# Optimization experiments

Measured on AMD Instinct MI355X. Metric: run time of the kernel, lower is better.

The kernel has to match this reference:

```python
import jax, jax.numpy as jnp
import numpy as np

NODELEN = 394
N_NODES = 50000
N_EDGES = 200000
IN_DIM = 2 * NODELEN  # 788
H2 = 192
EMB = 128


def setup_inputs() -> dict:
    key = jax.random.key(0)
    ks = jax.random.split(key, 12)
    inp = {
        'features': jax.random.normal(ks[0], (N_NODES, NODELEN), dtype=jnp.float32),
        'src': jax.random.randint(ks[1], (N_EDGES,), 0, N_NODES),
        'dst': jax.random.randint(ks[2], (N_EDGES,), 0, N_NODES),
        # AutoEncoder params (Linear weights stored as [in, out])
        'W_enc1': jax.random.normal(ks[3], (IN_DIM, H2), dtype=jnp.float32) / np.sqrt(IN_DIM),
        'b_enc1': jnp.zeros((H2,), dtype=jnp.float32),
        'W_enc3': jax.random.normal(ks[4], (H2, EMB), dtype=jnp.float32) / np.sqrt(H2),
        'b_enc3': jnp.zeros((EMB,), dtype=jnp.float32),
        'W_dec1': jax.random.normal(ks[5], (EMB, H2), dtype=jnp.float32) / np.sqrt(EMB),
        'b_dec1': jnp.zeros((H2,), dtype=jnp.float32),
        'W_dec3': jax.random.normal(ks[6], (H2, IN_DIM), dtype=jnp.float32) / np.sqrt(H2),
        'b_dec3': jnp.zeros((IN_DIM,), dtype=jnp.float32),
    }
    return inp


def _segment_mean(msgs, dst, inv_deg, n):
    # msgs: [E, F] gathered neighbor features; mean over incoming edges per node
    return jax.ops.segment_sum(msgs, dst, num_segments=n) * inv_deg


def reference(features, src, dst, W_enc1, b_enc1, W_enc3, b_enc3,
              W_dec1, b_dec1, W_dec3, b_dec3):
    n = features.shape[0]
    ones = jnp.ones(src.shape[0], dtype=features.dtype)
    deg = jax.ops.segment_sum(ones, dst, num_segments=n)
    # nodes with no neighbors fall back to the zero dummy vector (as in source)
    inv_deg = (1.0 / jnp.maximum(deg, 1.0))[:, None]

    # depth-1 aggregation: mean of raw neighbor features, then feat[0] := 0
    h1 = _segment_mean(features[src], dst, inv_deg, n)
    h1 = h1.at[:, 0].set(0.0)
    # depth-2 aggregation: mean of depth-1 aggregates of neighbors, feat[0] := 0
    h2 = _segment_mean(h1[src], dst, inv_deg, n)
    h2 = h2.at[:, 0].set(0.0)

    # concatenated embedding with positions 0 and NODELEN zeroed
    emb = jnp.concatenate([features, h2], axis=1)  # [N, 788]
    emb = emb.at[:, 0].set(0.0).at[:, NODELEN].set(0.0)

    # AutoEncoder forward (dropout is identity at inference)
    x = jax.nn.relu(emb @ W_enc1 + b_enc1)
    encoded = x @ W_enc3 + b_enc3
    y = jax.nn.relu(encoded @ W_dec1 + b_dec1)
    decoded = y @ W_dec3 + b_dec3
    return encoded, decoded, emb
```

## Files before the change

kernel.cpp:

```cpp
#include <hip/hip_runtime.h>
#include <hip/hip_bf16.h>

#define NODELEN 394
#define IN_DIM 788
#define H2DIM 192
#define EMBDIM 128
#define NCHUNK 197

typedef __attribute__((ext_vector_type(4))) float f32x4;
typedef __attribute__((ext_vector_type(8))) short bfrag;

static __device__ __forceinline__ unsigned short f2bf(float f) {
    union { float f; unsigned u; } v; v.f = f;
    unsigned r = v.u + 0x7FFFu + ((v.u >> 16) & 1u);
    return (unsigned short)(r >> 16);
}
static __device__ __forceinline__ float bf2f(unsigned short h) {
    union { unsigned u; float f; } v; v.u = ((unsigned)h) << 16;
    return v.f;
}


__global__ void count_deg(const int* __restrict__ dst, int* __restrict__ deg, int e) {
    int i = blockIdx.x * blockDim.x + threadIdx.x;
    if (i < e) atomicAdd(&deg[dst[i]], 1);
}

__global__ void block_sum(const int* __restrict__ deg, int* __restrict__ bsum, int n) {
    __shared__ int s[256];
    int t = threadIdx.x;
    int i = blockIdx.x * 256 + t;
    s[t] = (i < n) ? deg[i] : 0;
    __syncthreads();
    for (int d = 128; d > 0; d >>= 1) {
        if (t < d) s[t] += s[t + d];
        __syncthreads();
    }
    if (t == 0) bsum[blockIdx.x] = s[0];
}

__global__ void scan_bsums(int* bsum, int nb) {
    __shared__ int s[256];
    int t = threadIdx.x;
    int x0 = (t < nb) ? bsum[t] : 0;
    s[t] = x0;
    __syncthreads();
    for (int d = 1; d < 256; d <<= 1) {
        int u = (t >= d) ? s[t - d] : 0;
        __syncthreads();
        s[t] += u;
        __syncthreads();
    }
    if (t < nb) bsum[t] = s[t] - x0;
}

__global__ void block_scan(const int* __restrict__ deg, const int* __restrict__ boff,
                           int* __restrict__ rowstart, int* __restrict__ cursor,
                           float* __restrict__ inv, int n) {
    __shared__ int s[256];
    int t = threadIdx.x;
    int i = blockIdx.x * 256 + t;
    int x0 = (i < n) ? deg[i] : 0;
    s[t] = x0;
    __syncthreads();
    for (int d = 1; d < 256; d <<= 1) {
        int u = (t >= d) ? s[t - d] : 0;
        __syncthreads();
        s[t] += u;
        __syncthreads();
    }
    if (i < n) {
        int r = boff[blockIdx.x] + s[t] - x0;
        rowstart[i] = r;
        cursor[i] = r;
        inv[i] = 1.0f / fmaxf((float)x0, 1.0f);
    }
}

__global__ void fill_edges(const int* __restrict__ src, const int* __restrict__ dst,
                           int* __restrict__ cursor, int* __restrict__ elist, int e) {
    int i = blockIdx.x * blockDim.x + threadIdx.x;
    if (i < e) {
        int p = atomicAdd(&cursor[dst[i]], 1);
        elist[p] = src[i];
    }
}


__global__ __launch_bounds__(256) void gather1(
        const float* __restrict__ feat, const int* __restrict__ rowstart,
        const int* __restrict__ deg, const float* __restrict__ inv,
        const int* __restrict__ elist, unsigned short* __restrict__ h1) {
    const int node = blockIdx.x;
    const int c = threadIdx.x;
    if (c >= NCHUNK) return;
    const int beg = rowstart[node];
    const int dc = deg[node];
    const float s = inv[node];
    const size_t off = (size_t)c * 2;

    float ax = 0.f, ay = 0.f, bx = 0.f, by = 0.f;
    float cx = 0.f, cy = 0.f, dx = 0.f, dy = 0.f;
    int j = 0;
    for (; j + 3 < dc; j += 4) {
        int n0 = elist[beg + j], n1 = elist[beg + j + 1];
        int n2 = elist[beg + j + 2], n3 = elist[beg + j + 3];
        float2 v0 = *(const float2*)(feat + (size_t)n0 * NODELEN + off);
        float2 v1 = *(const float2*)(feat + (size_t)n1 * NODELEN + off);
        float2 v2 = *(const float2*)(feat + (size_t)n2 * NODELEN + off);
        float2 v3 = *(const float2*)(feat + (size_t)n3 * NODELEN + off);
        ax += v0.x; ay += v0.y; bx += v1.x; by += v1.y;
        cx += v2.x; cy += v2.y; dx += v3.x; dy += v3.y;
    }
    for (; j < dc; ++j) {
        int n0 = elist[beg + j];
        float2 v0 = *(const float2*)(feat + (size_t)n0 * NODELEN + off);
        ax += v0.x; ay += v0.y;
    }
    float fx = (ax + bx + cx + dx) * s;
    float fy = (ay + by + cy + dy) * s;
    if (c == 0) fx = 0.f;
    unsigned out = ((unsigned)f2bf(fy) << 16) | (unsigned)f2bf(fx);
    *(unsigned*)(h1 + (size_t)node * NODELEN + off) = out;
}

__global__ __launch_bounds__(256) void gather2_emb(
        const float* __restrict__ feat, const unsigned* __restrict__ h1,
        const int* __restrict__ rowstart, const int* __restrict__ deg,
        const float* __restrict__ inv, const int* __restrict__ elist,
        float* __restrict__ emb) {
    const int node = blockIdx.x;
    const int c = threadIdx.x;
    if (c >= NCHUNK) return;
    const int beg = rowstart[node];
    const int dc = deg[node];
    const float s = inv[node];

    float ax = 0.f, ay = 0.f, bx = 0.f, by = 0.f;
    float cx = 0.f, cy = 0.f, dx = 0.f, dy = 0.f;
    int j = 0;
    for (; j + 3 < dc; j += 4) {
        int n0 = elist[beg + j], n1 = elist[beg + j + 1];
        int n2 = elist[beg + j + 2], n3 = elist[beg + j + 3];
        unsigned u0 = h1[(size_t)n0 * NCHUNK + c];
        unsigned u1 = h1[(size_t)n1 * NCHUNK + c];
        unsigned u2 = h1[(size_t)n2 * NCHUNK + c];
        unsigned u3 = h1[(size_t)n3 * NCHUNK + c];
        ax += bf2f((unsigned short)u0); ay += bf2f((unsigned short)(u0 >> 16));
        bx += bf2f((unsigned short)u1); by += bf2f((unsigned short)(u1 >> 16));
        cx += bf2f((unsigned short)u2); cy += bf2f((unsigned short)(u2 >> 16));
        dx += bf2f((unsigned short)u3); dy += bf2f((unsigned short)(u3 >> 16));
    }
    for (; j < dc; ++j) {
        int n0 = elist[beg + j];
        unsigned u0 = h1[(size_t)n0 * NCHUNK + c];
        ax += bf2f((unsigned short)u0); ay += bf2f((unsigned short)(u0 >> 16));
    }
    float hx = (ax + bx + cx + dx) * s;
    float hy = (ay + by + cy + dy) * s;

    const float* fr = feat + (size_t)node * NODELEN;
    float* er = emb + (size_t)node * IN_DIM;
    float2 fv = *(const float2*)(fr + c * 2);
    if (c == 0) { fv.x = 0.f; hx = 0.f; }
    *(float2*)(er + c * 2) = fv;
    float2 hv; hv.x = hx; hv.y = hy;
    *(float2*)(er + NODELEN + c * 2) = hv;
}

__device__ __forceinline__ void tr_one(const float* W, unsigned short* Wt,
                                       int K, int N, int Kp, int idx) {
    int nrow = idx / Kp, k = idx - nrow * Kp;
    Wt[idx] = (k < K) ? f2bf(W[(size_t)k * N + nrow]) : (unsigned short)0;
}

#define T1E (192 * 800)
#define T2E (128 * 192)
#define T3E (192 * 128)
#define T4E (788 * 192)

__global__ void transpose_all(const float* __restrict__ W1, unsigned short* __restrict__ Wt1,
                              const float* __restrict__ W2, unsigned short* __restrict__ Wt2,
                              const float* __restrict__ W3, unsigned short* __restrict__ Wt3,
                              const float* __restrict__ W4, unsigned short* __restrict__ Wt4) {
    int idx = blockIdx.x * 256 + threadIdx.x;
    if (idx < T1E) { tr_one(W1, Wt1, IN_DIM, H2DIM, 800, idx); return; }
    idx -= T1E;
    if (idx < T2E) { tr_one(W2, Wt2, H2DIM, EMBDIM, 192, idx); return; }
    idx -= T2E;
    if (idx < T3E) { tr_one(W3, Wt3, EMBDIM, H2DIM, 128, idx); return; }
    idx -= T3E;
    if (idx < T4E) { tr_one(W4, Wt4, H2DIM, IN_DIM, 192, idx); return; }
}

static __device__ __forceinline__ int xy_base(int r, int s) {
    int ph = (s & 24) | ((s ^ r) & 7);
    return r * 192 + (ph << 3);
}
static __device__ __forceinline__ int xy_addr_s(int r, int col) { return xy_base(r, col >> 3) + (col & 7); }
static __device__ __forceinline__ int en_base(int r, int s) {
    int ph = (s & 8) | ((s ^ r) & 7);
    return r * 128 + (ph << 3);
}
static __device__ __forceinline__ int en_addr_s(int r, int col) { return en_base(r, col >> 3) + (col & 7); }

static __device__ __forceinline__ unsigned short f2bf_fast(float f) {
    __hip_bfloat16 h = __float2bfloat16(f);
    union { __hip_bfloat16 h; unsigned short u; } c; c.h = h; return c.u;
}

struct A8 { float4 a, b; };

static __device__ __forceinline__ void load_a(A8 out[2], const float* __restrict__ emb,
                                              int m0, int wm, int lr, int lk, int M, int kt) {
    int c = kt * 32 + lk * 8;
    #pragma unroll
    for (int i = 0; i < 2; ++i) {
        int gm = m0 + wm * 32 + i * 16 + lr;
        const float* rp = emb + (size_t)gm * IN_DIM;
        bool v = gm < M;
        if (v && c + 8 <= IN_DIM) {
            out[i].a = *(const float4*)(rp + c);
            out[i].b = *(const float4*)(rp + c + 4);
        } else {
            float t[8];
            #pragma unroll
            for (int q = 0; q < 8; ++q) t[q] = (v && c + q < IN_DIM) ? rp[c + q] : 0.f;
            out[i].a = make_float4(t[0], t[1], t[2], t[3]);
            out[i].b = make_float4(t[4], t[5], t[6], t[7]);
        }
    }
}

static __device__ __forceinline__ bfrag cvt_a(const A8& x) {
    union { unsigned short u[8]; bfrag v; } pk;
    pk.u[0] = f2bf_fast(x.a.x); pk.u[1] = f2bf_fast(x.a.y);
    pk.u[2] = f2bf_fast(x.a.z); pk.u[3] = f2bf_fast(x.a.w);
    pk.u[4] = f2bf_fast(x.b.x); pk.u[5] = f2bf_fast(x.b.y);
    pk.u[6] = f2bf_fast(x.b.z); pk.u[7] = f2bf_fast(x.b.w);
    return pk.v;
}

__global__ __launch_bounds__(256, 3) void mlp_fused(
    const float* __restrict__ emb,
    const unsigned short* __restrict__ Wt1,
    const unsigned short* __restrict__ Wt2,
    const unsigned short* __restrict__ Wt3,
    const unsigned short* __restrict__ Wt4,
    const float* __restrict__ b1, const float* __restrict__ b2,
    const float* __restrict__ b3, const float* __restrict__ b4,
    float* __restrict__ encoded, float* __restrict__ decoded, int M)
{
    __shared__ unsigned short XY[64 * 192];
    __shared__ unsigned short EN[64 * 128];

    const int tid = threadIdx.x;
    const int wid = tid >> 6, l = tid & 63;
    const int wm = wid >> 1, wn = wid & 1;
    const int lr = l & 15, lk = l >> 4;
    const int m0 = blockIdx.x * 64;
    const bfrag zf = {0, 0, 0, 0, 0, 0, 0, 0};

    {
        f32x4 acc[2][6];
        #pragma unroll
        for (int i = 0; i < 2; ++i)
            #pragma unroll
            for (int j = 0; j < 6; ++j) acc[i][j] = (f32x4){0.f, 0.f, 0.f, 0.f};

        const unsigned short* wp[6];
        #pragma unroll
        for (int j = 0; j < 6; ++j)
            wp[j] = Wt1 + (size_t)(wn * 96 + j * 16 + lr) * 800 + lk * 8;

        #pragma unroll 5
        for (int kt = 0; kt < 25; ++kt) {
            A8 a[2];
            load_a(a, emb, m0, wm, lr, lk, M, kt);
            bfrag bf[6];
            #pragma unroll
            for (int j = 0; j < 6; ++j) bf[j] = *(const bfrag*)(wp[j] + kt * 32);
            bfrag af0 = cvt_a(a[0]), af1 = cvt_a(a[1]);
            #pragma unroll
            for (int j = 0; j < 6; ++j) {
                acc[0][j] = __builtin_amdgcn_mfma_f32_16x16x32_bf16(af0, bf[j], acc[0][j], 0, 0, 0);
                acc[1][j] = __builtin_amdgcn_mfma_f32_16x16x32_bf16(af1, bf[j], acc[1][j], 0, 0, 0);
            }
        }
        float bv[6];
        #pragma unroll
        for (int j = 0; j < 6; ++j) bv[j] = b1[wn * 96 + j * 16 + lr];
        #pragma unroll
        for (int i = 0; i < 2; ++i)
            #pragma unroll
            for (int j = 0; j < 6; ++j)
                #pragma unroll
                for (int r = 0; r < 4; ++r) {
                    int m = wm * 32 + i * 16 + lk * 4 + r;
                    int n1 = wn * 96 + j * 16 + lr;
                    XY[xy_addr_s(m, n1)] = f2bf_fast(fmaxf(acc[i][j][r] + bv[j], 0.f));
                }
    }
    __syncthreads();

    {
        bfrag af2[6][2];
        #pragma unroll
        for (int q = 0; q < 6; ++q)
            #pragma unroll
            for (int i = 0; i < 2; ++i)
                af2[q][i] = *(const bfrag*)&XY[xy_base(wm * 32 + i * 16 + lr, q * 4 + lk)];

        f32x4 acc[2][4];
        #pragma unroll
        for (int i = 0; i < 2; ++i)
            #pragma unroll
            for (int j = 0; j < 4; ++j) acc[i][j] = (f32x4){0.f, 0.f, 0.f, 0.f};

        const unsigned short* wp[4];
        #pragma unroll
        for (int j = 0; j < 4; ++j)
            wp[j] = Wt2 + (size_t)(wn * 64 + j * 16 + lr) * 192 + lk * 8;

        #pragma unroll
        for (int kt = 0; kt < 6; ++kt) {
            bfrag bf[4];
            #pragma unroll
            for (int j = 0; j < 4; ++j) bf[j] = *(const bfrag*)(wp[j] + kt * 32);
            #pragma unroll
            for (int i = 0; i < 2; ++i)
                #pragma unroll
                for (int j = 0; j < 4; ++j)
                    acc[i][j] = __builtin_amdgcn_mfma_f32_16x16x32_bf16(af2[kt][i], bf[j], acc[i][j], 0, 0, 0);
        }
        float bv[4];
        #pragma unroll
        for (int j = 0; j < 4; ++j) bv[j] = b2[wn * 64 + j * 16 + lr];
        #pragma unroll
        for (int i = 0; i < 2; ++i)
            #pragma unroll
            for (int j = 0; j < 4; ++j)
                #pragma unroll
                for (int r = 0; r < 4; ++r) {
                    int m = wm * 32 + i * 16 + lk * 4 + r;
                    int nn = wn * 64 + j * 16 + lr;
                    float v = acc[i][j][r] + bv[j];
                    int gm = m0 + m;
                    if (gm < M) encoded[(size_t)gm * EMBDIM + nn] = v;
                    EN[en_addr_s(m, nn)] = f2bf_fast(v);
                }
    }
    __syncthreads();

    {
        bfrag af3[4][2];
        #pragma unroll
        for (int q = 0; q < 4; ++q)
            #pragma unroll
            for (int i = 0; i < 2; ++i)
                af3[q][i] = *(const bfrag*)&EN[en_base(wm * 32 + i * 16 + lr, q * 4 + lk)];

        f32x4 acc[2][6];
        #pragma unroll
        for (int i = 0; i < 2; ++i)
            #pragma unroll
            for (int j = 0; j < 6; ++j) acc[i][j] = (f32x4){0.f, 0.f, 0.f, 0.f};

        const unsigned short* wp[6];
        #pragma unroll
        for (int j = 0; j < 6; ++j)
            wp[j] = Wt3 + (size_t)(wn * 96 + j * 16 + lr) * 128 + lk * 8;

        #pragma unroll
        for (int kt = 0; kt < 4; ++kt) {
            bfrag bf[6];
            #pragma unroll
            for (int j = 0; j < 6; ++j) bf[j] = *(const bfrag*)(wp[j] + kt * 32);
            #pragma unroll
            for (int i = 0; i < 2; ++i)
                #pragma unroll
                for (int j = 0; j < 6; ++j)
                    acc[i][j] = __builtin_amdgcn_mfma_f32_16x16x32_bf16(af3[kt][i], bf[j], acc[i][j], 0, 0, 0);
        }
        float bv[6];
        #pragma unroll
        for (int j = 0; j < 6; ++j) bv[j] = b3[wn * 96 + j * 16 + lr];
        #pragma unroll
        for (int i = 0; i < 2; ++i)
            #pragma unroll
            for (int j = 0; j < 6; ++j)
                #pragma unroll
                for (int r = 0; r < 4; ++r) {
                    int m = wm * 32 + i * 16 + lk * 4 + r;
                    int nc = wn * 96 + j * 16 + lr;
                    XY[xy_addr_s(m, nc)] = f2bf_fast(fmaxf(acc[i][j][r] + bv[j], 0.f));
                }
    }
    __syncthreads();

    {
        bfrag af4[6][2];
        #pragma unroll
        for (int q = 0; q < 6; ++q)
            #pragma unroll
            for (int i = 0; i < 2; ++i)
                af4[q][i] = *(const bfrag*)&XY[xy_base(wm * 32 + i * 16 + lr, q * 4 + lk)];

        for (int nc = 0; nc < 7; ++nc) {
            f32x4 acc[2][4];
            #pragma unroll
            for (int i = 0; i < 2; ++i)
                #pragma unroll
                for (int j = 0; j < 4; ++j) acc[i][j] = (f32x4){0.f, 0.f, 0.f, 0.f};

            const int colb = nc * 128 + wn * 64 + lr;
            #pragma unroll
            for (int kt = 0; kt < 6; ++kt) {
                bfrag bf[4];
                #pragma unroll
                for (int j = 0; j < 4; ++j) {
                    int row = colb + j * 16;
                    bf[j] = (row < IN_DIM)
                        ? *(const bfrag*)(Wt4 + (size_t)row * 192 + kt * 32 + lk * 8) : zf;
                }
                #pragma unroll
                for (int i = 0; i < 2; ++i)
                    #pragma unroll
                    for (int j = 0; j < 4; ++j)
                        acc[i][j] = __builtin_amdgcn_mfma_f32_16x16x32_bf16(af4[kt][i], bf[j], acc[i][j], 0, 0, 0);
            }

            float bv[4];
            #pragma unroll
            for (int j = 0; j < 4; ++j) {
                int nn = colb + j * 16;
                bv[j] = (nn < IN_DIM) ? b4[nn] : 0.f;
            }
            #pragma unroll
            for (int i = 0; i < 2; ++i)
                #pragma unroll
                for (int j = 0; j < 4; ++j)
                    #pragma unroll
                    for (int r = 0; r < 4; ++r) {
                        int gm = m0 + wm * 32 + i * 16 + lk * 4 + r;
                        int nn = colb + j * 16;
                        if (gm < M && nn < IN_DIM)
                            decoded[(size_t)gm * IN_DIM + nn] = acc[i][j][r] + bv[j];
                    }
        }
    }
}


extern "C" void kernel_launch(void* const* d_in, const int* in_sizes, int n_in,
                              void* d_out, int out_size, void* d_ws, size_t ws_size,
                              hipStream_t stream) {
    const float* features = (const float*)d_in[0];
    const int*   src      = (const int*)d_in[1];
    const int*   dst      = (const int*)d_in[2];
    const float* W_enc1   = (const float*)d_in[3];
    const float* b_enc1   = (const float*)d_in[4];
    const float* W_enc3   = (const float*)d_in[5];
    const float* b_enc3   = (const float*)d_in[6];
    const float* W_dec1   = (const float*)d_in[7];
    const float* b_dec1   = (const float*)d_in[8];
    const float* W_dec3   = (const float*)d_in[9];
    const float* b_dec3   = (const float*)d_in[10];

    const int n = in_sizes[0] / NODELEN;
    const int e = in_sizes[1];

    float* encoded = (float*)d_out;
    float* decoded = encoded + (size_t)n * EMBDIM;
    float* emb     = decoded + (size_t)n * IN_DIM;

    char* ws = (char*)d_ws;
    unsigned short* h1  = (unsigned short*)(ws + 0);
    unsigned short* Wt1 = (unsigned short*)(ws + 40000000);
    unsigned short* Wt2 = (unsigned short*)(ws + 40400000);
    unsigned short* Wt3 = (unsigned short*)(ws + 40500000);
    unsigned short* Wt4 = (unsigned short*)(ws + 40600000);
    float* inv          = (float*)(ws + 41000000);
    int*   deg          = (int*)  (ws + 41200000);
    int*   rowstart     = (int*)  (ws + 41400000);
    int*   cursor       = (int*)  (ws + 41600000);
    int*   elist        = (int*)  (ws + 41800000);
    int*   bsum         = (int*)  (ws + 42600000);

    const int nb = (n + 255) / 256;
    const int eb = (e + 255) / 256;

    transpose_all<<<(T1E + T2E + T3E + T4E + 255) / 256, 256, 0, stream>>>(
        W_enc1, Wt1, W_enc3, Wt2, W_dec1, Wt3, W_dec3, Wt4);

    hipMemsetAsync(deg, 0, (size_t)n * sizeof(int), stream);
    count_deg<<<eb, 256, 0, stream>>>(dst, deg, e);
    block_sum<<<nb, 256, 0, stream>>>(deg, bsum, n);
    scan_bsums<<<1, 256, 0, stream>>>(bsum, nb);
    block_scan<<<nb, 256, 0, stream>>>(deg, bsum, rowstart, cursor, inv, n);
    fill_edges<<<eb, 256, 0, stream>>>(src, dst, cursor, elist, e);

    gather1<<<n, 256, 0, stream>>>(features, rowstart, deg, inv, elist, h1);
    gather2_emb<<<n, 256, 0, stream>>>(features, (const unsigned*)h1, rowstart, deg,
                                       inv, elist, emb);

    const int MB = (n + 63) / 64;
    mlp_fused<<<MB, 256, 0, stream>>>(emb, Wt1, Wt2, Wt3, Wt4,
                                      b_enc1, b_enc3, b_dec1, b_dec3,
                                      encoded, decoded, n);
}
```

Measured before the change: 415.3 us.

## Split fused MLP into two kernels and stage weights through double-buffered LDS

```diff
diff --git a/kernel.cpp b/kernel.cpp
--- a/kernel.cpp
+++ b/kernel.cpp
@@ -193,16 +193,14 @@
     if (idx < T4E) { tr_one(W4, Wt4, H2DIM, IN_DIM, 192, idx); return; }
 }
 
+static __device__ __forceinline__ int bs_addr(int r, int s) {
+    return r * 32 + ((s ^ ((r >> 1) & 3)) << 3);
+}
 static __device__ __forceinline__ int xy_base(int r, int s) {
     int ph = (s & 24) | ((s ^ r) & 7);
     return r * 192 + (ph << 3);
 }
 static __device__ __forceinline__ int xy_addr_s(int r, int col) { return xy_base(r, col >> 3) + (col & 7); }
-static __device__ __forceinline__ int en_base(int r, int s) {
-    int ph = (s & 8) | ((s ^ r) & 7);
-    return r * 128 + (ph << 3);
-}
-static __device__ __forceinline__ int en_addr_s(int r, int col) { return en_base(r, col >> 3) + (col & 7); }
 
 static __device__ __forceinline__ unsigned short f2bf_fast(float f) {
     __hip_bfloat16 h = __float2bfloat16(f);
@@ -241,18 +239,162 @@
     return pk.v;
 }
 
-__global__ __launch_bounds__(256, 3) void mlp_fused(
+__global__ __launch_bounds__(256, 3) void mlp12(
     const float* __restrict__ emb,
     const unsigned short* __restrict__ Wt1,
     const unsigned short* __restrict__ Wt2,
+    const float* __restrict__ b1, const float* __restrict__ b2,
+    float* __restrict__ encoded, unsigned short* __restrict__ enc16, int M)
+{
+    __shared__ unsigned short XY[64 * 192];
+    __shared__ unsigned short Bs[2][192 * 32];
+
+    const int tid = threadIdx.x;
+    const int wid = tid >> 6, l = tid & 63;
+    const int wm = wid >> 1, wn = wid & 1;
+    const int lr = l & 15, lk = l >> 4;
+    const int m0 = blockIdx.x * 64;
+
+    const int r0 = tid >> 2, s0 = tid & 3;
+    const int r1 = (tid + 256) >> 2;
+    const int r2 = (tid + 512) >> 2;
+    const int bw0 = bs_addr(r0, s0);
+    const int bw1 = bs_addr(r1, s0);
+    const int bw2 = bs_addr(r2, s0);
+    int brd6[6], brd4[4];
+    #pragma unroll
+    for (int j = 0; j < 6; ++j) brd6[j] = bs_addr(wn * 96 + j * 16 + lr, lk);
+    #pragma unroll
+    for (int j = 0; j < 4; ++j) brd4[j] = bs_addr(wn * 64 + j * 16 + lr, lk);
+
+    {
+        f32x4 acc[2][6];
+        #pragma unroll
+        for (int i = 0; i < 2; ++i)
+            #pragma unroll
+            for (int j = 0; j < 6; ++j) acc[i][j] = (f32x4){0.f, 0.f, 0.f, 0.f};
+
+        A8 aC[2], aN[2];
+        bfrag bC[3], bN[3];
+        load_a(aC, emb, m0, wm, lr, lk, M, 0);
+        bC[0] = *(const bfrag*)(Wt1 + (size_t)r0 * 800 + s0 * 8);
+        bC[1] = *(const bfrag*)(Wt1 + (size_t)r1 * 800 + s0 * 8);
+        bC[2] = *(const bfrag*)(Wt1 + (size_t)r2 * 800 + s0 * 8);
+
+        #pragma unroll 5
+        for (int kt = 0; kt < 25; ++kt) {
+            unsigned short* B = Bs[kt & 1];
+            *(bfrag*)&B[bw0] = bC[0];
+            *(bfrag*)&B[bw1] = bC[1];
+            *(bfrag*)&B[bw2] = bC[2];
+            if (kt < 24) {
+                int k0 = (kt + 1) * 32;
+                load_a(aN, emb, m0, wm, lr, lk, M, kt + 1);
+                bN[0] = *(const bfrag*)(Wt1 + (size_t)r0 * 800 + k0 + s0 * 8);
+                bN[1] = *(const bfrag*)(Wt1 + (size_t)r1 * 800 + k0 + s0 * 8);
+                bN[2] = *(const bfrag*)(Wt1 + (size_t)r2 * 800 + k0 + s0 * 8);
+            }
+            __syncthreads();
+            bfrag af0 = cvt_a(aC[0]), af1 = cvt_a(aC[1]);
+            bfrag bf[6];
+            #pragma unroll
+            for (int j = 0; j < 6; ++j) bf[j] = *(const bfrag*)&B[brd6[j]];
+            #pragma unroll
+            for (int j = 0; j < 6; ++j) {
+                acc[0][j] = __builtin_amdgcn_mfma_f32_16x16x32_bf16(af0, bf[j], acc[0][j], 0, 0, 0);
+                acc[1][j] = __builtin_amdgcn_mfma_f32_16x16x32_bf16(af1, bf[j], acc[1][j], 0, 0, 0);
+            }
+            if (kt < 24) {
+                aC[0] = aN[0]; aC[1] = aN[1];
+                bC[0] = bN[0]; bC[1] = bN[1]; bC[2] = bN[2];
+            }
+        }
+        float bv[6];
+        #pragma unroll
+        for (int j = 0; j < 6; ++j) bv[j] = b1[wn * 96 + j * 16 + lr];
+        #pragma unroll
+        for (int i = 0; i < 2; ++i)
+            #pragma unroll
+            for (int j = 0; j < 6; ++j)
+                #pragma unroll
+                for (int r = 0; r < 4; ++r) {
+                    int m = wm * 32 + i * 16 + lk * 4 + r;
+                    int n1 = wn * 96 + j * 16 + lr;
+                    XY[xy_addr_s(m, n1)] = f2bf_fast(fmaxf(acc[i][j][r] + bv[j], 0.f));
+                }
+    }
+    __syncthreads();
+
+    {
+        bfrag af2[6][2];
+        #pragma unroll
+        for (int q = 0; q < 6; ++q)
+            #pragma unroll
+            for (int i = 0; i < 2; ++i)
+                af2[q][i] = *(const bfrag*)&XY[xy_base(wm * 32 + i * 16 + lr, q * 4 + lk)];
+
+        f32x4 acc[2][4];
+        #pragma unroll
+        for (int i = 0; i < 2; ++i)
+            #pragma unroll
+            for (int j = 0; j < 4; ++j) acc[i][j] = (f32x4){0.f, 0.f, 0.f, 0.f};
+
+        bfrag bC[2], bN[2];
+        bC[0] = *(const bfrag*)(Wt2 + (size_t)r0 * 192 + s0 * 8);
+        bC[1] = *(const bfrag*)(Wt2 + (size_t)r1 * 192 + s0 * 8);
+
+        #pragma unroll
+        for (int kt = 0; kt < 6; ++kt) {
+            unsigned short* B = Bs[kt & 1];
+            *(bfrag*)&B[bw0] = bC[0];
+            *(bfrag*)&B[bw1] = bC[1];
+            if (kt < 5) {
+                int k0 = (kt + 1) * 32;
+                bN[0] = *(const bfrag*)(Wt2 + (size_t)r0 * 192 + k0 + s0 * 8);
+                bN[1] = *(const bfrag*)(Wt2 + (size_t)r1 * 192 + k0 + s0 * 8);
+            }
+            __syncthreads();
+            bfrag bf[4];
+            #pragma unroll
+            for (int j = 0; j < 4; ++j) bf[j] = *(const bfrag*)&B[brd4[j]];
+            #pragma unroll
+            for (int i = 0; i < 2; ++i)
+                #pragma unroll
+                for (int j = 0; j < 4; ++j)
+                    acc[i][j] = __builtin_amdgcn_mfma_f32_16x16x32_bf16(af2[kt][i], bf[j], acc[i][j], 0, 0, 0);
+            if (kt < 5) { bC[0] = bN[0]; bC[1] = bN[1]; }
+        }
+
+        float bv[4];
+        #pragma unroll
+        for (int j = 0; j < 4; ++j) bv[j] = b2[wn * 64 + j * 16 + lr];
+        #pragma unroll
+        for (int i = 0; i < 2; ++i)
+            #pragma unroll
+            for (int j = 0; j < 4; ++j)
+                #pragma unroll
+                for (int r = 0; r < 4; ++r) {
+                    int m = wm * 32 + i * 16 + lk * 4 + r;
+                    int nn = wn * 64 + j * 16 + lr;
+                    float v = acc[i][j][r] + bv[j];
+                    int gm = m0 + m;
+                    if (gm < M) {
+                        encoded[(size_t)gm * EMBDIM + nn] = v;
+                        enc16[(size_t)gm * EMBDIM + nn] = f2bf_fast(v);
+                    }
+                }
+    }
+}
+
+__global__ __launch_bounds__(256, 3) void mlp34(
+    const unsigned short* __restrict__ enc16,
     const unsigned short* __restrict__ Wt3,
     const unsigned short* __restrict__ Wt4,
-    const float* __restrict__ b1, const float* __restrict__ b2,
     const float* __restrict__ b3, const float* __restrict__ b4,
-    float* __restrict__ encoded, float* __restrict__ decoded, int M)
+    float* __restrict__ decoded, int M)
 {
     __shared__ unsigned short XY[64 * 192];
-    __shared__ unsigned short EN[64 * 128];
+    __shared__ unsigned short Bs[2][192 * 32];
 
     const int tid = threadIdx.x;
     const int wid = tid >> 6, l = tid & 63;
@@ -261,104 +403,26 @@
     const int m0 = blockIdx.x * 64;
     const bfrag zf = {0, 0, 0, 0, 0, 0, 0, 0};
 
-    {
-        f32x4 acc[2][6];
-        #pragma unroll
-        for (int i = 0; i < 2; ++i)
-            #pragma unroll
-            for (int j = 0; j < 6; ++j) acc[i][j] = (f32x4){0.f, 0.f, 0.f, 0.f};
-
-        const unsigned short* wp[6];
-        #pragma unroll
-        for (int j = 0; j < 6; ++j)
-            wp[j] = Wt1 + (size_t)(wn * 96 + j * 16 + lr) * 800 + lk * 8;
-
-        #pragma unroll 5
-        for (int kt = 0; kt < 25; ++kt) {
-            A8 a[2];
-            load_a(a, emb, m0, wm, lr, lk, M, kt);
-            bfrag bf[6];
-            #pragma unroll
-            for (int j = 0; j < 6; ++j) bf[j] = *(const bfrag*)(wp[j] + kt * 32);
-            bfrag af0 = cvt_a(a[0]), af1 = cvt_a(a[1]);
-            #pragma unroll
-            for (int j = 0; j < 6; ++j) {
-                acc[0][j] = __builtin_amdgcn_mfma_f32_16x16x32_bf16(af0, bf[j], acc[0][j], 0, 0, 0);
-                acc[1][j] = __builtin_amdgcn_mfma_f32_16x16x32_bf16(af1, bf[j], acc[1][j], 0, 0, 0);
-            }
-        }
-        float bv[6];
-        #pragma unroll
-        for (int j = 0; j < 6; ++j) bv[j] = b1[wn * 96 + j * 16 + lr];
-        #pragma unroll
-        for (int i = 0; i < 2; ++i)
-            #pragma unroll
-            for (int j = 0; j < 6; ++j)
-                #pragma unroll
-                for (int r = 0; r < 4; ++r) {
-                    int m = wm * 32 + i * 16 + lk * 4 + r;
-                    int n1 = wn * 96 + j * 16 + lr;
-                    XY[xy_addr_s(m, n1)] = f2bf_fast(fmaxf(acc[i][j][r] + bv[j], 0.f));
-                }
-    }
-    __syncthreads();
-
-    {
-        bfrag af2[6][2];
-        #pragma unroll
-        for (int q = 0; q < 6; ++q)
-            #pragma unroll
-            for (int i = 0; i < 2; ++i)
-                af2[q][i] = *(const bfrag*)&XY[xy_base(wm * 32 + i * 16 + lr, q * 4 + lk)];
-
-        f32x4 acc[2][4];
-        #pragma unroll
-        for (int i = 0; i < 2; ++i)
-            #pragma unroll
-            for (int j = 0; j < 4; ++j) acc[i][j] = (f32x4){0.f, 0.f, 0.f, 0.f};
-
-        const unsigned short* wp[4];
-        #pragma unroll
-        for (int j = 0; j < 4; ++j)
-            wp[j] = Wt2 + (size_t)(wn * 64 + j * 16 + lr) * 192 + lk * 8;
-
-        #pragma unroll
-        for (int kt = 0; kt < 6; ++kt) {
-            bfrag bf[4];
-            #pragma unroll
-            for (int j = 0; j < 4; ++j) bf[j] = *(const bfrag*)(wp[j] + kt * 32);
-            #pragma unroll
-            for (int i = 0; i < 2; ++i)
-                #pragma unroll
-                for (int j = 0; j < 4; ++j)
-                    acc[i][j] = __builtin_amdgcn_mfma_f32_16x16x32_bf16(af2[kt][i], bf[j], acc[i][j], 0, 0, 0);
-        }
-        float bv[4];
-        #pragma unroll
-        for (int j = 0; j < 4; ++j) bv[j] = b2[wn * 64 + j * 16 + lr];
-        #pragma unroll
-        for (int i = 0; i < 2; ++i)
-            #pragma unroll
-            for (int j = 0; j < 4; ++j)
-                #pragma unroll
-                for (int r = 0; r < 4; ++r) {
-                    int m = wm * 32 + i * 16 + lk * 4 + r;
-                    int nn = wn * 64 + j * 16 + lr;
-                    float v = acc[i][j][r] + bv[j];
-                    int gm = m0 + m;
-                    if (gm < M) encoded[(size_t)gm * EMBDIM + nn] = v;
-                    EN[en_addr_s(m, nn)] = f2bf_fast(v);
-                }
-    }
-    __syncthreads();
+    const int r0 = tid >> 2, s0 = tid & 3;
+    const int r1 = (tid + 256) >> 2;
+    const int r2 = (tid + 512) >> 2;
+    const int bw0 = bs_addr(r0, s0);
+    const int bw1 = bs_addr(r1, s0);
+    const int bw2 = bs_addr(r2, s0);
+    int brd6[6];
+    #pragma unroll
+    for (int j = 0; j < 6; ++j) brd6[j] = bs_addr(wn * 96 + j * 16 + lr, lk);
 
     {
         bfrag af3[4][2];
         #pragma unroll
         for (int q = 0; q < 4; ++q)
             #pragma unroll
-            for (int i = 0; i < 2; ++i)
-                af3[q][i] = *(const bfrag*)&EN[en_base(wm * 32 + i * 16 + lr, q * 4 + lk)];
+            for (int i = 0; i < 2; ++i) {
+                int gm = m0 + wm * 32 + i * 16 + lr;
+                af3[q][i] = (gm < M)
+                    ? *(const bfrag*)(enc16 + (size_t)gm * EMBDIM + q * 32 + lk * 8) : zf;
+            }
 
         f32x4 acc[2][6];
         #pragma unroll
@@ -366,22 +430,35 @@
             #pragma unroll
             for (int j = 0; j < 6; ++j) acc[i][j] = (f32x4){0.f, 0.f, 0.f, 0.f};
 
-        const unsigned short* wp[6];
-        #pragma unroll
-        for (int j = 0; j < 6; ++j)
-            wp[j] = Wt3 + (size_t)(wn * 96 + j * 16 + lr) * 128 + lk * 8;
+        bfrag bC[3], bN[3];
+        bC[0] = *(const bfrag*)(Wt3 + (size_t)r0 * 128 + s0 * 8);
+        bC[1] = *(const bfrag*)(Wt3 + (size_t)r1 * 128 + s0 * 8);
+        bC[2] = *(const bfrag*)(Wt3 + (size_t)r2 * 128 + s0 * 8);
 
         #pragma unroll
         for (int kt = 0; kt < 4; ++kt) {
+            unsigned short* B = Bs[kt & 1];
+            *(bfrag*)&B[bw0] = bC[0];
+            *(bfrag*)&B[bw1] = bC[1];
+            *(bfrag*)&B[bw2] = bC[2];
+            if (kt < 3) {
+                int k0 = (kt + 1) * 32;
+                bN[0] = *(const bfrag*)(Wt3 + (size_t)r0 * 128 + k0 + s0 * 8);
+                bN[1] = *(const bfrag*)(Wt3 + (size_t)r1 * 128 + k0 + s0 * 8);
+                bN[2] = *(const bfrag*)(Wt3 + (size_t)r2 * 128 + k0 + s0 * 8);
+            }
+            __syncthreads();
             bfrag bf[6];
             #pragma unroll
-            for (int j = 0; j < 6; ++j) bf[j] = *(const bfrag*)(wp[j] + kt * 32);
+            for (int j = 0; j < 6; ++j) bf[j] = *(const bfrag*)&B[brd6[j]];
             #pragma unroll
             for (int i = 0; i < 2; ++i)
                 #pragma unroll
                 for (int j = 0; j < 6; ++j)
                     acc[i][j] = __builtin_amdgcn_mfma_f32_16x16x32_bf16(af3[kt][i], bf[j], acc[i][j], 0, 0, 0);
+            if (kt < 3) { bC[0] = bN[0]; bC[1] = bN[1]; bC[2] = bN[2]; }
         }
+
         float bv[6];
         #pragma unroll
         for (int j = 0; j < 6; ++j) bv[j] = b3[wn * 96 + j * 16 + lr];
@@ -406,44 +483,59 @@
             for (int i = 0; i < 2; ++i)
                 af4[q][i] = *(const bfrag*)&XY[xy_base(wm * 32 + i * 16 + lr, q * 4 + lk)];
 
-        for (int nc = 0; nc < 7; ++nc) {
-            f32x4 acc[2][4];
+        bfrag bC[3], bN[3];
+        bC[0] = *(const bfrag*)(Wt4 + (size_t)r0 * 192 + s0 * 8);
+        bC[1] = *(const bfrag*)(Wt4 + (size_t)r1 * 192 + s0 * 8);
+        bC[2] = *(const bfrag*)(Wt4 + (size_t)r2 * 192 + s0 * 8);
+
+        for (int nc = 0; nc < 5; ++nc) {
+            f32x4 acc[2][6];
             #pragma unroll
             for (int i = 0; i < 2; ++i)
                 #pragma unroll
-                for (int j = 0; j < 4; ++j) acc[i][j] = (f32x4){0.f, 0.f, 0.f, 0.f};
-
-            const int colb = nc * 128 + wn * 64 + lr;
+                for (int j = 0; j < 6; ++j) acc[i][j] = (f32x4){0.f, 0.f, 0.f, 0.f};
+
             #pragma unroll
             for (int kt = 0; kt < 6; ++kt) {
-                bfrag bf[4];
-                #pragma unroll
-                for (int j = 0; j < 4; ++j) {
-                    int row = colb + j * 16;
-                    bf[j] = (row < IN_DIM)
-                        ? *(const bfrag*)(Wt4 + (size_t)row * 192 + kt * 32 + lk * 8) : zf;
+                const int t = nc * 6 + kt;
+                unsigned short* B = Bs[t & 1];
+                *(bfrag*)&B[bw0] = bC[0];
+                *(bfrag*)&B[bw1] = bC[1];
+                *(bfrag*)&B[bw2] = bC[2];
+                if (t < 29) {
+                    int nn = (kt < 5) ? nc : nc + 1;
+                    int nk = (kt < 5) ? (kt + 1) * 32 : 0;
+                    int g0 = nn * 192 + r0, g1 = nn * 192 + r1, g2 = nn * 192 + r2;
+                    bN[0] = (g0 < IN_DIM) ? *(const bfrag*)(Wt4 + (size_t)g0 * 192 + nk + s0 * 8) : zf;
+                    bN[1] = (g1 < IN_DIM) ? *(const bfrag*)(Wt4 + (size_t)g1 * 192 + nk + s0 * 8) : zf;
+                    bN[2] = (g2 < IN_DIM) ? *(const bfrag*)(Wt4 + (size_t)g2 * 192 + nk + s0 * 8) : zf;
                 }
+                __syncthreads();
+                bfrag bf[6];
+                #pragma unroll
+                for (int j = 0; j < 6; ++j) bf[j] = *(const bfrag*)&B[brd6[j]];
                 #pragma unroll
                 for (int i = 0; i < 2; ++i)
                     #pragma unroll
-                    for (int j = 0; j < 4; ++j)
+                    for (int j = 0; j < 6; ++j)
                         acc[i][j] = __builtin_amdgcn_mfma_f32_16x16x32_bf16(af4[kt][i], bf[j], acc[i][j], 0, 0, 0);
-            }
-
-            float bv[4];
-            #pragma unroll
-            for (int j = 0; j < 4; ++j) {
-                int nn = colb + j * 16;
+                bC[0] = bN[0]; bC[1] = bN[1]; bC[2] = bN[2];
+            }
+
+            float bv[6];
+            #pragma unroll
+            for (int j = 0; j < 6; ++j) {
+                int nn = nc * 192 + wn * 96 + j * 16 + lr;
                 bv[j] = (nn < IN_DIM) ? b4[nn] : 0.f;
             }
             #pragma unroll
             for (int i = 0; i < 2; ++i)
                 #pragma unroll
-                for (int j = 0; j < 4; ++j)
+                for (int j = 0; j < 6; ++j)
                     #pragma unroll
                     for (int r = 0; r < 4; ++r) {
                         int gm = m0 + wm * 32 + i * 16 + lk * 4 + r;
-                        int nn = colb + j * 16;
+                        int nn = nc * 192 + wn * 96 + j * 16 + lr;
                         if (gm < M && nn < IN_DIM)
                             decoded[(size_t)gm * IN_DIM + nn] = acc[i][j][r] + bv[j];
                     }
@@ -475,7 +567,8 @@
     float* emb     = decoded + (size_t)n * IN_DIM;
 
     char* ws = (char*)d_ws;
-    unsigned short* h1  = (unsigned short*)(ws + 0);
+    unsigned short* h1    = (unsigned short*)(ws + 0);
+    unsigned short* enc16 = (unsigned short*)(ws + 0);
     unsigned short* Wt1 = (unsigned short*)(ws + 40000000);
     unsigned short* Wt2 = (unsigned short*)(ws + 40400000);
     unsigned short* Wt3 = (unsigned short*)(ws + 40500000);
@@ -505,7 +598,6 @@
                                        inv, elist, emb);
 
     const int MB = (n + 63) / 64;
-    mlp_fused<<<MB, 256, 0, stream>>>(emb, Wt1, Wt2, Wt3, Wt4,
-                                      b_enc1, b_enc3, b_dec1, b_dec3,
-                                      encoded, decoded, n);
-}
+    mlp12<<<MB, 256, 0, stream>>>(emb, Wt1, Wt2, b_enc1, b_enc3, encoded, enc16, n);
+    mlp34<<<MB, 256, 0, stream>>>(enc16, Wt3, Wt4, b_dec1, b_dec3, decoded, n);
+}
```

After: 350.7 us. 15.6% less time.
